# Kernel optimization log

Hardware: AMD Instinct MI355X
Metric: run time of the kernel (lower is better)

The kernel has to match this reference:

```python
import jax, jax.numpy as jnp
import numpy as np

B_, H_, W_, C_ = 8, 56, 56, 96
D_ = int(C_ * 2.0)          # d_inner = 192
N_ = 16                     # d_state
K_ = 4                      # scan directions
R_ = (C_ + 15) // 16        # dt_rank 'auto' = 6
MLP_H = 4 * C_
EPS = 1e-5


def setup_inputs() -> dict:
    key = jax.random.key(0)
    ks = jax.random.split(key, 16)
    s = 0.02
    rn = lambda k, sh, sc=1.0: jax.random.normal(k, sh, dtype=jnp.float32) * sc
    return dict(
        x=rn(ks[0], (B_, H_, W_, C_)),
        ln1_w=jnp.ones((C_,), jnp.float32), ln1_b=jnp.zeros((C_,), jnp.float32),
        in_proj_w=rn(ks[1], (2 * D_, C_), s),
        conv_w=rn(ks[2], (D_, 1, 3, 3), s), conv_b=jnp.zeros((D_,), jnp.float32),
        x_proj_w=rn(ks[3], (K_, R_ + 2 * N_, D_), s),
        dt_proj_w=rn(ks[4], (K_, D_, R_), s),
        dt_proj_b=rn(ks[5], (K_, D_), 0.1),
        A_logs=jax.random.uniform(ks[6], (K_ * D_, N_), jnp.float32, 0.0, 3.0),
        Ds=jnp.ones((K_ * D_,), jnp.float32),
        out_norm_w=jnp.ones((D_,), jnp.float32), out_norm_b=jnp.zeros((D_,), jnp.float32),
        out_proj_w=rn(ks[7], (C_, D_), s),
        ln2_w=jnp.ones((C_,), jnp.float32), ln2_b=jnp.zeros((C_,), jnp.float32),
        fc1_w=rn(ks[8], (MLP_H, C_), s), fc1_b=jnp.zeros((MLP_H,), jnp.float32),
        fc2_w=rn(ks[9], (C_, MLP_H), s), fc2_b=jnp.zeros((C_,), jnp.float32),
    )


def layer_norm(x, w, b):
    m = x.mean(-1, keepdims=True)
    v = ((x - m) ** 2).mean(-1, keepdims=True)
    return (x - m) / jnp.sqrt(v + EPS) * w + b


def ss2d(x, in_proj_w, conv_w, conv_b, x_proj_w, dt_proj_w, dt_proj_b,
         A_logs, Ds, out_norm_w, out_norm_b, out_proj_w):
    Bn, Hh, Ww, C = x.shape
    L = Hh * Ww
    xz = x @ in_proj_w.T                       # (B,H,W,2D)
    xc, z = jnp.split(xz, 2, axis=-1)
    xc = xc.transpose(0, 3, 1, 2)              # (B,D,H,W)
    xc = jax.lax.conv_general_dilated(xc, conv_w, (1, 1), 'SAME',
                                      feature_group_count=D_)
    xc = jax.nn.silu(xc + conv_b[None, :, None, None])
    # cross-scan: 4 traversal orders, each (B,D,L)
    x0 = xc.reshape(Bn, D_, L)
    x1 = xc.transpose(0, 1, 3, 2).reshape(Bn, D_, L)
    xs = jnp.stack([x0, x1, x0[..., ::-1], x1[..., ::-1]], axis=1)  # (B,K,D,L)
    xdbl = jnp.einsum('bkdl,kcd->bkcl', xs, x_proj_w)
    dts, Bs, Cs = jnp.split(xdbl, [R_, R_ + N_], axis=2)            # (B,K,R,L),(B,K,N,L)x2
    dts = jnp.einsum('bkrl,kdr->bkdl', dts, dt_proj_w)
    dts = jax.nn.softplus(dts + dt_proj_b[None, :, :, None])        # (B,K,D,L)
    A = -jnp.exp(A_logs).reshape(K_, D_, N_)                        # (K,D,N)

    def step(h, inp):
        xt, dtt, Bt, Ct = inp                  # (B,K,D),(B,K,D),(B,K,N),(B,K,N)
        h = h * jnp.exp(dtt[..., None] * A) + (dtt * xt)[..., None] * Bt[:, :, None, :]
        return h, jnp.einsum('bkdn,bkn->bkd', h, Ct)

    inps = (xs.transpose(3, 0, 1, 2), dts.transpose(3, 0, 1, 2),
            Bs.transpose(3, 0, 1, 2), Cs.transpose(3, 0, 1, 2))
    h0 = jnp.zeros((Bn, K_, D_, N_), jnp.float32)
    _, ys = jax.lax.scan(step, h0, inps)       # (L,B,K,D)
    ys = ys.transpose(1, 2, 3, 0)              # (B,K,D,L)
    ys = ys + Ds.reshape(K_, D_)[None, :, :, None] * xs
    # cross-merge: undo flips and transposed order
    y = ys[:, 0] + ys[:, 2, :, ::-1]
    y = y + (ys[:, 1] + ys[:, 3, :, ::-1]).reshape(Bn, D_, Ww, Hh) \
            .transpose(0, 1, 3, 2).reshape(Bn, D_, L)
    y = y.transpose(0, 2, 1).reshape(Bn, Hh, Ww, D_)
    y = layer_norm(y, out_norm_w, out_norm_b)
    y = y * jax.nn.silu(z)
    return y @ out_proj_w.T


def reference(x, ln1_w, ln1_b, in_proj_w, conv_w, conv_b, x_proj_w, dt_proj_w,
              dt_proj_b, A_logs, Ds, out_norm_w, out_norm_b, out_proj_w,
              ln2_w, ln2_b, fc1_w, fc1_b, fc2_w, fc2_b):
    # norm -> SS2D -> residual
    x = x + ss2d(layer_norm(x, ln1_w, ln1_b), in_proj_w, conv_w, conv_b,
                 x_proj_w, dt_proj_w, dt_proj_b, A_logs, Ds,
                 out_norm_w, out_norm_b, out_proj_w)
    # norm -> MLP -> residual
    h = layer_norm(x, ln2_w, ln2_b)
    h = jax.nn.gelu(h @ fc1_w.T + fc1_b) @ fc2_w.T + fc2_b
    return x + h
```

## Files before the change

kernel.cpp:

```cpp
#include <hip/hip_runtime.h>
#include <hip/hip_bf16.h>

typedef __hip_bfloat16 bf16;
typedef short bf16x8 __attribute__((ext_vector_type(8)));
typedef float f32x4 __attribute__((ext_vector_type(4)));

#define BBATCH 8
#define HHH 56
#define WWW 56
#define CCH 96
#define DIN 192
#define NST 16
#define KDIR 4
#define RDT 6
#define LLEN 3136
#define BLTOT 25088
#define SSEG 64
#define SEGL 49
#define PJC 38
#define PJW 152
#define PJS 40
#define PJS1 24
#define MLPH 384

#if defined(__has_builtin)
#if __has_builtin(__builtin_amdgcn_exp2f)
#define EXP2F(x) __builtin_amdgcn_exp2f(x)
#endif
#if __has_builtin(__builtin_amdgcn_logf)
#define LOG2F_(x) __builtin_amdgcn_logf(x)
#endif
#endif
#ifndef EXP2F
#define EXP2F(x) __expf((x) * 0.69314718056f)
#endif
#ifndef LOG2F_
#define LOG2F_(x) (__logf(x) * 1.44269504f)
#endif
#define LOG2E 1.44269504f

__device__ __forceinline__ float2 pk_mul(float2 a, float2 b) {
    float2 d;
    asm("v_pk_mul_f32 %0, %1, %2" : "=v"(d) : "v"(a), "v"(b));
    return d;
}
__device__ __forceinline__ float2 pk_fma(float2 a, float2 b, float2 c) {
    float2 d;
    asm("v_pk_fma_f32 %0, %1, %2, %3" : "=v"(d) : "v"(a), "v"(b), "v"(c));
    return d;
}

__device__ __forceinline__ float b2f(bf16 v) { return __bfloat162float(v); }
__device__ __forceinline__ bf16  f2b(float v) { return __float2bfloat16(v); }
__device__ __forceinline__ unsigned short f2bu(float f) {
    union { bf16 h; unsigned short u; } c; c.h = __float2bfloat16(f); return c.u;
}
__device__ __forceinline__ float bu2f(unsigned short u) {
    union { unsigned short u; bf16 h; } c; c.u = u; return __bfloat162float(c.h);
}
__device__ __forceinline__ float sigm(float x) { return 1.f / (1.f + __expf(-x)); }
__device__ __forceinline__ float softplusf(float x) {
    float t = EXP2F(-fabsf(x) * LOG2E);
    return fmaxf(x, 0.f) + 0.69314718f * LOG2F_(1.f + t);
}
__device__ __forceinline__ float geluf(float v) {
    float u = 0.7978845608028654f * (v + 0.044715f * v * v * v);
    float ey = __expf(2.f * u);
    float th = 1.f - 2.f / (ey + 1.f);
    return 0.5f * v * (1.f + th);
}

__device__ __forceinline__ int pos_map(int k, int l) {
    if (k & 2) l = LLEN - 1 - l;
    if (k & 1) { int q = l / WWW; int r = l - q * WWW; return r * WWW + q; }
    return l;
}

__global__ __launch_bounds__(256) void ln_rows(
    const float* __restrict__ xin, const float* __restrict__ w,
    const float* __restrict__ b, unsigned short* __restrict__ xn) {
    int row = blockIdx.x * 4 + (threadIdx.x >> 6);
    int lane = threadIdx.x & 63;
    const float* xr = xin + (size_t)row * 96;
    float2 v = make_float2(0.f, 0.f);
    if (lane < 48) v = *(const float2*)&xr[lane * 2];
    float s = v.x + v.y, s2 = v.x * v.x + v.y * v.y;
    for (int o = 32; o; o >>= 1) {
        s += __shfl_down(s, o);
        s2 += __shfl_down(s2, o);
    }
    s = __shfl(s, 0); s2 = __shfl(s2, 0);
    float m = s * (1.f / 96.f);
    float var = s2 * (1.f / 96.f) - m * m;
    float rs = rsqrtf(var + 1e-5f);
    if (lane < 48) {
        float o0 = (v.x - m) * rs * w[lane * 2] + b[lane * 2];
        float o1 = (v.y - m) * rs * w[lane * 2 + 1] + b[lane * 2 + 1];
        ushort2 u; u.x = f2bu(o0); u.y = f2bu(o1);
        *(ushort2*)&xn[(size_t)row * 96 + lane * 2] = u;
    }
}

template<int N, int K, int EPI>
__global__ __launch_bounds__(256) void gemm_mfma(
    const unsigned short* __restrict__ X, const float* __restrict__ W,
    const float* __restrict__ bias, const float* __restrict__ res,
    void* __restrict__ out0v, void* __restrict__ out1v) {
    __shared__ unsigned short a_sh[128 * 40];
    __shared__ unsigned short b_sh[64 * 40];
    const int t = threadIdx.x;
    const int P0 = blockIdx.x * 128;
    const int N0 = blockIdx.y * 64;
    const int w = t >> 6, lane = t & 63, q = lane >> 4, nl = lane & 15;
    f32x4 acc[2][4];
#pragma unroll
    for (int i = 0; i < 2; ++i)
#pragma unroll
        for (int j = 0; j < 4; ++j)
            acc[i][j] = (f32x4){0.f, 0.f, 0.f, 0.f};
    for (int k0 = 0; k0 < K; k0 += 32) {
        __syncthreads();
#pragma unroll
        for (int it = 0; it < 2; ++it) {
            int idx = t + it * 256;
            int pr = idx >> 2, kq = idx & 3;
            uint4 v = *(const uint4*)&X[(size_t)(P0 + pr) * K + k0 + kq * 8];
            *(uint4*)&a_sh[pr * 40 + kq * 8] = v;
        }
#pragma unroll
        for (int it = 0; it < 2; ++it) {
            int idx = t + it * 256;
            int nr = idx >> 3, kq = idx & 7;
            int ng = N0 + nr; if (ng > N - 1) ng = N - 1;
            float4 v = *(const float4*)&W[(size_t)ng * K + k0 + kq * 4];
            ushort4 u;
            u.x = f2bu(v.x); u.y = f2bu(v.y); u.z = f2bu(v.z); u.w = f2bu(v.w);
            *(ushort4*)&b_sh[nr * 40 + kq * 4] = u;
        }
        __syncthreads();
        bf16x8 af[2], bfr[4];
#pragma unroll
        for (int mf = 0; mf < 2; ++mf)
            af[mf] = *(const bf16x8*)&a_sh[(w * 32 + mf * 16 + nl) * 40 + q * 8];
#pragma unroll
        for (int nf = 0; nf < 4; ++nf)
            bfr[nf] = *(const bf16x8*)&b_sh[(nf * 16 + nl) * 40 + q * 8];
#pragma unroll
        for (int mf = 0; mf < 2; ++mf)
#pragma unroll
            for (int nf = 0; nf < 4; ++nf)
                acc[mf][nf] = __builtin_amdgcn_mfma_f32_16x16x32_bf16(
                    af[mf], bfr[nf], acc[mf][nf], 0, 0, 0);
    }
#pragma unroll
    for (int mf = 0; mf < 2; ++mf) {
#pragma unroll
        for (int nf = 0; nf < 4; ++nf) {
#pragma unroll
            for (int r = 0; r < 4; ++r) {
                float v = acc[mf][nf][r];
                size_t pos = (size_t)P0 + w * 32 + mf * 16 + q * 4 + r;
                int n = N0 + nf * 16 + nl;
                if constexpr (EPI == 0) {
                    unsigned short* xc = (unsigned short*)out0v;
                    unsigned short* zz = (unsigned short*)out1v;
                    if (n < 192) xc[pos * 192 + n] = f2bu(v);
                    else         zz[pos * 192 + (n - 192)] = f2bu(v);
                } else if constexpr (EPI == 1) {
                    if (n < 152) ((float*)out0v)[pos * 152 + n] = v;
                } else if constexpr (EPI == 2) {
                    if (n < 96) ((float*)out0v)[pos * 96 + n] = res[pos * 96 + n] + v;
                } else if constexpr (EPI == 3) {
                    ((unsigned short*)out0v)[pos * 384 + n] = f2bu(geluf(v + bias[n]));
                } else {
                    if (n < 96) ((float*)out0v)[pos * 96 + n] =
                        res[pos * 96 + n] + bias[n] + v;
                }
            }
        }
    }
}

__global__ __launch_bounds__(256) void k2_conv(
    const unsigned short* __restrict__ xcpre, const float* __restrict__ cw,
    const float* __restrict__ cb, unsigned short* __restrict__ xconv) {
    int idx = blockIdx.x * 256 + threadIdx.x;
    int dd = idx % 48;
    int P = idx / 48;
    int d0 = dd * 4;
    int b = P / LLEN, l = P - b * LLEN;
    int h = l / WWW, w = l - h * WWW;
    float acc0 = cb[d0], acc1 = cb[d0 + 1], acc2 = cb[d0 + 2], acc3 = cb[d0 + 3];
#pragma unroll
    for (int i = 0; i < 3; ++i) {
        int hh = h + i - 1;
        if (hh < 0 || hh >= HHH) continue;
#pragma unroll
        for (int j = 0; j < 3; ++j) {
            int ww = w + j - 1;
            if (ww < 0 || ww >= WWW) continue;
            ushort4 xv = *(const ushort4*)&xcpre[
                ((size_t)(b * LLEN + hh * WWW + ww)) * DIN + d0];
            acc0 = fmaf(bu2f(xv.x), cw[(d0 + 0) * 9 + i * 3 + j], acc0);
            acc1 = fmaf(bu2f(xv.y), cw[(d0 + 1) * 9 + i * 3 + j], acc1);
            acc2 = fmaf(bu2f(xv.z), cw[(d0 + 2) * 9 + i * 3 + j], acc2);
            acc3 = fmaf(bu2f(xv.w), cw[(d0 + 3) * 9 + i * 3 + j], acc3);
        }
    }
    acc0 = acc0 * sigm(acc0); acc1 = acc1 * sigm(acc1);
    acc2 = acc2 * sigm(acc2); acc3 = acc3 * sigm(acc3);
    ushort4 o;
    o.x = f2bu(acc0); o.y = f2bu(acc1); o.z = f2bu(acc2); o.w = f2bu(acc3);
    *(ushort4*)&xconv[(size_t)P * DIN + d0] = o;
}

__global__ __launch_bounds__(192) void k4_scan1(
    const bf16* __restrict__ xconv, const float* __restrict__ proj,
    const float* __restrict__ dtw, const float* __restrict__ dtb,
    const float* __restrict__ Alog, float* __restrict__ hloc,
    float* __restrict__ tsum) {
    __shared__ float pl[SEGL * PJS1];
    __shared__ int posl[SEGL];
    const int bid = blockIdx.x;
    const int s = bid & 63, k = (bid >> 6) & 3, b = bid >> 8;
    const int d = threadIdx.x;
    const int l0 = s * SEGL;
    for (int q = d; q < SEGL * 22; q += 192) {
        int st = q / 22, c = q - st * 22;
        int p = pos_map(k, l0 + st);
        int ofs = (c < 6) ? c : c + 2;
        pl[st * PJS1 + ofs] = proj[(size_t)(b * LLEN + p) * PJW + k * PJC + c];
    }
    if (d < SEGL) posl[d] = pos_map(k, l0 + d) * DIN;
    float w6[RDT];
#pragma unroll
    for (int r = 0; r < RDT; ++r) w6[r] = dtw[(k * DIN + d) * RDT + r];
    const float bias = dtb[k * DIN + d];
    float2 a2[8];
#pragma unroll
    for (int j = 0; j < 8; ++j) {
        a2[j].x = -__expf(Alog[(k * DIN + d) * NST + 2 * j]) * LOG2E;
        a2[j].y = -__expf(Alog[(k * DIN + d) * NST + 2 * j + 1]) * LOG2E;
    }
    float2 h2[8];
#pragma unroll
    for (int j = 0; j < 8; ++j) h2[j] = make_float2(0.f, 0.f);
    float T = 0.f;
    __syncthreads();
    const bf16* xg = xconv + (size_t)b * LLEN * DIN + d;
    for (int bt = 0; bt < 7; ++bt) {
        int off7[7]; float xv7[7];
#pragma unroll
        for (int i = 0; i < 7; ++i) off7[i] = posl[bt * 7 + i];
#pragma unroll
        for (int i = 0; i < 7; ++i) xv7[i] = b2f(xg[off7[i]]);
#pragma unroll
        for (int i = 0; i < 7; ++i) {
            const float* rowf = &pl[(bt * 7 + i) * PJS1];
            float4 g0 = *(const float4*)(rowf);
            float2 g1 = *(const float2*)(rowf + 4);
            float dtv = bias;
            dtv = fmaf(g0.x, w6[0], dtv); dtv = fmaf(g0.y, w6[1], dtv);
            dtv = fmaf(g0.z, w6[2], dtv); dtv = fmaf(g0.w, w6[3], dtv);
            dtv = fmaf(g1.x, w6[4], dtv); dtv = fmaf(g1.y, w6[5], dtv);
            dtv = softplusf(dtv);
            T += dtv;
            float2 dt2 = make_float2(dtv, dtv);
            float2 u2 = make_float2(dtv * xv7[i], dtv * xv7[i]);
#pragma unroll
            for (int g = 0; g < 4; ++g) {
                float4 Bv = *(const float4*)(rowf + 8 + 4 * g);
                float2 Blo = make_float2(Bv.x, Bv.y);
                float2 Bhi = make_float2(Bv.z, Bv.w);
                float2 alo = pk_mul(dt2, a2[2 * g]);
                float2 ahi = pk_mul(dt2, a2[2 * g + 1]);
                float2 elo, ehi;
                elo.x = EXP2F(alo.x); elo.y = EXP2F(alo.y);
                ehi.x = EXP2F(ahi.x); ehi.y = EXP2F(ahi.y);
                h2[2 * g]     = pk_fma(h2[2 * g],     elo, pk_mul(u2, Blo));
                h2[2 * g + 1] = pk_fma(h2[2 * g + 1], ehi, pk_mul(u2, Bhi));
            }
        }
    }
    size_t base = ((size_t)bid * DIN + d) * NST;
#pragma unroll
    for (int j = 0; j < 8; ++j) *(float2*)&hloc[base + 2 * j] = h2[j];
    tsum[bid * DIN + d] = T;
}

__global__ __launch_bounds__(256) void k5_carry(
    const float* hloc, const float* __restrict__ tsum,
    const float* __restrict__ Alog, float* hin) {
    int g = blockIdx.x * 256 + threadIdx.x;
    int n = g & 15;
    int dk = g >> 4;
    int d = dk % DIN;
    int bk = dk / DIN;
    int k = bk & 3;
    float a2 = -__expf(Alog[(k * DIN + d) * NST + n]) * LOG2E;
    float Hc = 0.f;
    for (int s = 0; s < SSEG; ++s) {
        int bid = bk * SSEG + s;
        size_t idx = ((size_t)bid * DIN + d) * NST + n;
        float hl = hloc[idx];
        float Tv = tsum[bid * DIN + d];
        hin[idx] = Hc;
        Hc = fmaf(EXP2F(a2 * Tv), Hc, hl);
    }
}

__global__ __launch_bounds__(192) void k6_scan2(
    const bf16* __restrict__ xconv, const float* __restrict__ proj,
    const float* __restrict__ dtw, const float* __restrict__ dtb,
    const float* __restrict__ Alog, const float* __restrict__ Dsp,
    const float* __restrict__ hin, bf16* __restrict__ ysm) {
    __shared__ float pl[SEGL * PJS];
    __shared__ int posl[SEGL];
    const int bid = blockIdx.x;
    const int s = bid & 63, k = (bid >> 6) & 3, b = bid >> 8;
    const int d = threadIdx.x;
    const int l0 = s * SEGL;
    for (int q = d; q < SEGL * PJC; q += 192) {
        int st = q / PJC, c = q - st * PJC;
        int p = pos_map(k, l0 + st);
        int ofs = (c < 6) ? c : c + 2;
        pl[st * PJS + ofs] = proj[(size_t)(b * LLEN + p) * PJW + k * PJC + c];
    }
    if (d < SEGL) posl[d] = pos_map(k, l0 + d) * DIN;
    float w6[RDT];
#pragma unroll
    for (int r = 0; r < RDT; ++r) w6[r] = dtw[(k * DIN + d) * RDT + r];
    const float bias = dtb[k * DIN + d];
    const float dsv = Dsp[k * DIN + d];
    float2 a2[8];
#pragma unroll
    for (int j = 0; j < 8; ++j) {
        a2[j].x = -__expf(Alog[(k * DIN + d) * NST + 2 * j]) * LOG2E;
        a2[j].y = -__expf(Alog[(k * DIN + d) * NST + 2 * j + 1]) * LOG2E;
    }
    float2 h2[8];
    size_t hbase = ((size_t)bid * DIN + d) * NST;
#pragma unroll
    for (int j = 0; j < 8; ++j) h2[j] = *(const float2*)&hin[hbase + 2 * j];
    __syncthreads();
    const bf16* xg = xconv + (size_t)b * LLEN * DIN + d;
    bf16* ysg = ysm + ((size_t)(b * KDIR + k) * LLEN) * DIN + d;
    for (int bt = 0; bt < 7; ++bt) {
        int off7[7]; float xv7[7];
#pragma unroll
        for (int i = 0; i < 7; ++i) off7[i] = posl[bt * 7 + i];
#pragma unroll
        for (int i = 0; i < 7; ++i) xv7[i] = b2f(xg[off7[i]]);
#pragma unroll
        for (int i = 0; i < 7; ++i) {
            const float* rowf = &pl[(bt * 7 + i) * PJS];
            float4 g0 = *(const float4*)(rowf);
            float2 g1 = *(const float2*)(rowf + 4);
            float dtv = bias;
            dtv = fmaf(g0.x, w6[0], dtv); dtv = fmaf(g0.y, w6[1], dtv);
            dtv = fmaf(g0.z, w6[2], dtv); dtv = fmaf(g0.w, w6[3], dtv);
            dtv = fmaf(g1.x, w6[4], dtv); dtv = fmaf(g1.y, w6[5], dtv);
            dtv = softplusf(dtv);
            float2 dt2 = make_float2(dtv, dtv);
            float2 u2 = make_float2(dtv * xv7[i], dtv * xv7[i]);
            float2 yac0 = make_float2(0.f, 0.f), yac1 = make_float2(0.f, 0.f);
#pragma unroll
            for (int g = 0; g < 4; ++g) {
                float4 Bv = *(const float4*)(rowf + 8 + 4 * g);
                float4 Cv = *(const float4*)(rowf + 24 + 4 * g);
                float2 Blo = make_float2(Bv.x, Bv.y);
                float2 Bhi = make_float2(Bv.z, Bv.w);
                float2 Clo = make_float2(Cv.x, Cv.y);
                float2 Chi = make_float2(Cv.z, Cv.w);
                float2 alo = pk_mul(dt2, a2[2 * g]);
                float2 ahi = pk_mul(dt2, a2[2 * g + 1]);
                float2 elo, ehi;
                elo.x = EXP2F(alo.x); elo.y = EXP2F(alo.y);
                ehi.x = EXP2F(ahi.x); ehi.y = EXP2F(ahi.y);
                h2[2 * g]     = pk_fma(h2[2 * g],     elo, pk_mul(u2, Blo));
                h2[2 * g + 1] = pk_fma(h2[2 * g + 1], ehi, pk_mul(u2, Bhi));
                yac0 = pk_fma(h2[2 * g],     Clo, yac0);
                yac1 = pk_fma(h2[2 * g + 1], Chi, yac1);
            }
            float y = (yac0.x + yac0.y) + (yac1.x + yac1.y);
            ysg[off7[i]] = f2b(fmaf(dsv, xv7[i], y));
        }
    }
}

__global__ __launch_bounds__(256) void k65_merge(
    const bf16* __restrict__ ysm, const bf16* __restrict__ z,
    const float* __restrict__ onw, const float* __restrict__ onb,
    bf16* __restrict__ ymod) {
    __shared__ float rb[16 * DIN];
    __shared__ float ps[256], pq[256];
    __shared__ float mrow[16], srow[16];
    const int t = threadIdx.x;
    const int P0 = blockIdx.x * 16;
    for (int q = t; q < 16 * DIN; q += 256) {
        int pos = q / DIN, c = q - pos * DIN;
        int P = P0 + pos;
        int b = P / LLEN, l = P - b * LLEN;
        size_t base = ((size_t)(b * KDIR) * LLEN + l) * DIN + c;
        size_t pstr = (size_t)LLEN * DIN;
        float v = b2f(ysm[base]) + b2f(ysm[base + pstr]) +
                  b2f(ysm[base + 2 * pstr]) + b2f(ysm[base + 3 * pstr]);
        rb[q] = v;
    }
    __syncthreads();
    {
        int pos = t >> 4, part = t & 15;
        float s = 0.f, s2 = 0.f;
        for (int i = 0; i < 12; ++i) {
            float v = rb[pos * DIN + part * 12 + i];
            s += v; s2 += v * v;
        }
        ps[pos * 16 + part] = s; pq[pos * 16 + part] = s2;
    }
    __syncthreads();
    if (t < 16) {
        float s = 0.f, s2 = 0.f;
        for (int i = 0; i < 16; ++i) { s += ps[t * 16 + i]; s2 += pq[t * 16 + i]; }
        float m = s * (1.f / DIN);
        float v = s2 * (1.f / DIN) - m * m;
        mrow[t] = m; srow[t] = rsqrtf(v + 1e-5f);
    }
    __syncthreads();
    for (int q = t; q < 16 * DIN; q += 256) {
        int pos = q / DIN, c = q - pos * DIN;
        int P = P0 + pos;
        float v = (rb[q] - mrow[pos]) * srow[pos] * onw[c] + onb[c];
        float zv = b2f(z[(size_t)P * DIN + c]);
        v *= zv * sigm(zv);
        ymod[(size_t)P * DIN + c] = f2b(v);
    }
}

extern "C" void kernel_launch(void* const* d_in, const int* in_sizes, int n_in,
                              void* d_out, int out_size, void* d_ws, size_t ws_size,
                              hipStream_t stream) {
    const float* x      = (const float*)d_in[0];
    const float* ln1w   = (const float*)d_in[1];
    const float* ln1b   = (const float*)d_in[2];
    const float* inpW   = (const float*)d_in[3];
    const float* convW  = (const float*)d_in[4];
    const float* convB  = (const float*)d_in[5];
    const float* xprojW = (const float*)d_in[6];
    const float* dtW    = (const float*)d_in[7];
    const float* dtB    = (const float*)d_in[8];
    const float* Alog   = (const float*)d_in[9];
    const float* Dsp    = (const float*)d_in[10];
    const float* onw    = (const float*)d_in[11];
    const float* onb    = (const float*)d_in[12];
    const float* outW   = (const float*)d_in[13];
    const float* ln2w   = (const float*)d_in[14];
    const float* ln2b   = (const float*)d_in[15];
    const float* fc1W   = (const float*)d_in[16];
    const float* fc1b   = (const float*)d_in[17];
    const float* fc2W   = (const float*)d_in[18];
    const float* fc2b   = (const float*)d_in[19];
    float* out = (float*)d_out;

    char* ws = (char*)d_ws;
    unsigned short* z_us    = (unsigned short*)(ws + 0);
    bf16*  z_bf             = (bf16*)z_us;
    bf16*  xconv_bf         = (bf16*)(ws + 9633792);
    float* proj_f           = (float*)(ws + 19267584);
    bf16*  ymod_bf          = (bf16*)(ws + 19267584);
    unsigned short* xn_us   = (unsigned short*)(ws + 34521088);
    float* tsum_f           = (float*)(ws + 34521088);
    unsigned short* xcpre_us= (unsigned short*)(ws + 39337984);
    float* hloc_f           = (float*)(ws + 48971776);
    float* hin_f            = hloc_f;
    float* y1_f             = (float*)(ws + 48971776);
    unsigned short* y1n_us  = (unsigned short*)(ws + 58605568);
    bf16*  ysm_bf           = (bf16*)(ws + 74137600);
    unsigned short* hmlp_us = (unsigned short*)(ws + 74137600);

    ln_rows<<<6272, 256, 0, stream>>>(x, ln1w, ln1b, xn_us);
    gemm_mfma<384, 96, 0><<<dim3(196, 6), 256, 0, stream>>>(
        xn_us, inpW, nullptr, nullptr, xcpre_us, z_us);
    k2_conv<<<4704, 256, 0, stream>>>(xcpre_us, convW, convB,
                                      (unsigned short*)xconv_bf);
    gemm_mfma<152, 192, 1><<<dim3(196, 3), 256, 0, stream>>>(
        (const unsigned short*)xconv_bf, xprojW, nullptr, nullptr, proj_f, nullptr);
    k4_scan1<<<2048, 192, 0, stream>>>(xconv_bf, proj_f, dtW, dtB, Alog, hloc_f, tsum_f);
    k5_carry<<<384, 256, 0, stream>>>(hloc_f, tsum_f, Alog, hin_f);
    k6_scan2<<<2048, 192, 0, stream>>>(xconv_bf, proj_f, dtW, dtB, Alog, Dsp, hin_f, ysm_bf);
    k65_merge<<<1568, 256, 0, stream>>>(ysm_bf, z_bf, onw, onb, ymod_bf);
    gemm_mfma<96, 192, 2><<<dim3(196, 2), 256, 0, stream>>>(
        (const unsigned short*)ymod_bf, outW, nullptr, x, y1_f, nullptr);
    ln_rows<<<6272, 256, 0, stream>>>(y1_f, ln2w, ln2b, y1n_us);
    gemm_mfma<384, 96, 3><<<dim3(196, 6), 256, 0, stream>>>(
        y1n_us, fc1W, fc1b, nullptr, hmlp_us, nullptr);
    gemm_mfma<96, 384, 4><<<dim3(196, 2), 256, 0, stream>>>(
        hmlp_us, fc2W, fc2b, y1_f, out, nullptr);
}
```

Measured before the change: 387.2 us.

## Split scan into more shorter segments and precompute A coefficients once

Raises the number of chunked-scan segments per sequence from 64 to 112 (28 steps each), so the two scan passes launch 3584 blocks instead of 2048 and fill more compute units with a shorter serial chain per block. A small pre-kernel computes -exp(A_log)*log2e once into workspace, and the scan and carry kernels load it instead of recomputing exponentials. Workspace offsets are reshuffled to fit the larger per-segment state buffers. In exchange, the serial carry kernel runs longer (112 steps) and the hloc/hin traffic grows with the segment count.

Result: faster. 379.5 us (-2.0%).

```diff
diff --git a/kernel.cpp b/kernel.cpp
--- a/kernel.cpp
+++ b/kernel.cpp
@@ -15,8 +15,8 @@
 #define RDT 6
 #define LLEN 3136
 #define BLTOT 25088
-#define SSEG 64
-#define SEGL 49
+#define SSEG 112
+#define SEGL 28
 #define PJC 38
 #define PJW 152
 #define PJS 40
@@ -74,6 +74,12 @@
     if (k & 2) l = LLEN - 1 - l;
     if (k & 1) { int q = l / WWW; int r = l - q * WWW; return r * WWW + q; }
     return l;
+}
+
+__global__ __launch_bounds__(256) void k0_pre(
+    const float* __restrict__ Alog, float* __restrict__ a2g) {
+    int i = blockIdx.x * 256 + threadIdx.x;
+    a2g[i] = -__expf(Alog[i]) * LOG2E;
 }
 
 __global__ __launch_bounds__(256) void ln_rows(
@@ -217,12 +223,14 @@
 __global__ __launch_bounds__(192) void k4_scan1(
     const bf16* __restrict__ xconv, const float* __restrict__ proj,
     const float* __restrict__ dtw, const float* __restrict__ dtb,
-    const float* __restrict__ Alog, float* __restrict__ hloc,
+    const float* __restrict__ a2g, float* __restrict__ hloc,
     float* __restrict__ tsum) {
     __shared__ float pl[SEGL * PJS1];
     __shared__ int posl[SEGL];
     const int bid = blockIdx.x;
-    const int s = bid & 63, k = (bid >> 6) & 3, b = bid >> 8;
+    const int s = bid % SSEG;
+    const int bk = bid / SSEG;
+    const int k = bk & 3, b = bk >> 2;
     const int d = threadIdx.x;
     const int l0 = s * SEGL;
     for (int q = d; q < SEGL * 22; q += 192) {
@@ -238,17 +246,15 @@
     const float bias = dtb[k * DIN + d];
     float2 a2[8];
 #pragma unroll
-    for (int j = 0; j < 8; ++j) {
-        a2[j].x = -__expf(Alog[(k * DIN + d) * NST + 2 * j]) * LOG2E;
-        a2[j].y = -__expf(Alog[(k * DIN + d) * NST + 2 * j + 1]) * LOG2E;
-    }
+    for (int j = 0; j < 8; ++j)
+        a2[j] = *(const float2*)&a2g[(k * DIN + d) * NST + 2 * j];
     float2 h2[8];
 #pragma unroll
     for (int j = 0; j < 8; ++j) h2[j] = make_float2(0.f, 0.f);
     float T = 0.f;
     __syncthreads();
     const bf16* xg = xconv + (size_t)b * LLEN * DIN + d;
-    for (int bt = 0; bt < 7; ++bt) {
+    for (int bt = 0; bt < 4; ++bt) {
         int off7[7]; float xv7[7];
 #pragma unroll
         for (int i = 0; i < 7; ++i) off7[i] = posl[bt * 7 + i];
@@ -290,14 +296,14 @@
 
 __global__ __launch_bounds__(256) void k5_carry(
     const float* hloc, const float* __restrict__ tsum,
-    const float* __restrict__ Alog, float* hin) {
+    const float* __restrict__ a2g, float* hin) {
     int g = blockIdx.x * 256 + threadIdx.x;
     int n = g & 15;
     int dk = g >> 4;
     int d = dk % DIN;
     int bk = dk / DIN;
     int k = bk & 3;
-    float a2 = -__expf(Alog[(k * DIN + d) * NST + n]) * LOG2E;
+    float a2 = a2g[(k * DIN + d) * NST + n];
     float Hc = 0.f;
     for (int s = 0; s < SSEG; ++s) {
         int bid = bk * SSEG + s;
@@ -312,12 +318,14 @@
 __global__ __launch_bounds__(192) void k6_scan2(
     const bf16* __restrict__ xconv, const float* __restrict__ proj,
     const float* __restrict__ dtw, const float* __restrict__ dtb,
-    const float* __restrict__ Alog, const float* __restrict__ Dsp,
+    const float* __restrict__ a2g, const float* __restrict__ Dsp,
     const float* __restrict__ hin, bf16* __restrict__ ysm) {
     __shared__ float pl[SEGL * PJS];
     __shared__ int posl[SEGL];
     const int bid = blockIdx.x;
-    const int s = bid & 63, k = (bid >> 6) & 3, b = bid >> 8;
+    const int s = bid % SSEG;
+    const int bk = bid / SSEG;
+    const int k = bk & 3, b = bk >> 2;
     const int d = threadIdx.x;
     const int l0 = s * SEGL;
     for (int q = d; q < SEGL * PJC; q += 192) {
@@ -334,18 +342,16 @@
     const float dsv = Dsp[k * DIN + d];
     float2 a2[8];
 #pragma unroll
-    for (int j = 0; j < 8; ++j) {
-        a2[j].x = -__expf(Alog[(k * DIN + d) * NST + 2 * j]) * LOG2E;
-        a2[j].y = -__expf(Alog[(k * DIN + d) * NST + 2 * j + 1]) * LOG2E;
-    }
+    for (int j = 0; j < 8; ++j)
+        a2[j] = *(const float2*)&a2g[(k * DIN + d) * NST + 2 * j];
     float2 h2[8];
     size_t hbase = ((size_t)bid * DIN + d) * NST;
 #pragma unroll
     for (int j = 0; j < 8; ++j) h2[j] = *(const float2*)&hin[hbase + 2 * j];
     __syncthreads();
     const bf16* xg = xconv + (size_t)b * LLEN * DIN + d;
-    bf16* ysg = ysm + ((size_t)(b * KDIR + k) * LLEN) * DIN + d;
-    for (int bt = 0; bt < 7; ++bt) {
+    bf16* ysg = ysm + ((size_t)bk * LLEN) * DIN + d;
+    for (int bt = 0; bt < 4; ++bt) {
         int off7[7]; float xv7[7];
 #pragma unroll
         for (int i = 0; i < 7; ++i) off7[i] = posl[bt * 7 + i];
@@ -470,13 +476,15 @@
     unsigned short* xn_us   = (unsigned short*)(ws + 34521088);
     float* tsum_f           = (float*)(ws + 34521088);
     unsigned short* xcpre_us= (unsigned short*)(ws + 39337984);
-    float* hloc_f           = (float*)(ws + 48971776);
+    float* hloc_f           = (float*)(ws + 39337984);
     float* hin_f            = hloc_f;
-    float* y1_f             = (float*)(ws + 48971776);
-    unsigned short* y1n_us  = (unsigned short*)(ws + 58605568);
-    bf16*  ysm_bf           = (bf16*)(ws + 74137600);
-    unsigned short* hmlp_us = (unsigned short*)(ws + 74137600);
-
+    float* y1_f             = (float*)(ws + 39337984);
+    unsigned short* y1n_us  = (unsigned short*)(ws + 48971776);
+    bf16*  ysm_bf           = (bf16*)(ws + 83378176);
+    unsigned short* hmlp_us = (unsigned short*)(ws + 83378176);
+    float* a2g_f            = (float*)(ws + 121913344);
+
+    k0_pre<<<48, 256, 0, stream>>>(Alog, a2g_f);
     ln_rows<<<6272, 256, 0, stream>>>(x, ln1w, ln1b, xn_us);
     gemm_mfma<384, 96, 0><<<dim3(196, 6), 256, 0, stream>>>(
         xn_us, inpW, nullptr, nullptr, xcpre_us, z_us);
@@ -484,9 +492,11 @@
                                       (unsigned short*)xconv_bf);
     gemm_mfma<152, 192, 1><<<dim3(196, 3), 256, 0, stream>>>(
         (const unsigned short*)xconv_bf, xprojW, nullptr, nullptr, proj_f, nullptr);
-    k4_scan1<<<2048, 192, 0, stream>>>(xconv_bf, proj_f, dtW, dtB, Alog, hloc_f, tsum_f);
-    k5_carry<<<384, 256, 0, stream>>>(hloc_f, tsum_f, Alog, hin_f);
-    k6_scan2<<<2048, 192, 0, stream>>>(xconv_bf, proj_f, dtW, dtB, Alog, Dsp, hin_f, ysm_bf);
+    k4_scan1<<<3584, 192, 0, stream>>>(xconv_bf, proj_f, dtW, dtB, a2g_f,
+                                       hloc_f, tsum_f);
+    k5_carry<<<384, 256, 0, stream>>>(hloc_f, tsum_f, a2g_f, hin_f);
+    k6_scan2<<<3584, 192, 0, stream>>>(xconv_bf, proj_f, dtW, dtB, a2g_f, Dsp,
+                                       hin_f, ysm_bf);
     k65_merge<<<1568, 256, 0, stream>>>(ysm_bf, z_bf, onw, onb, ymod_bf);
     gemm_mfma<96, 192, 2><<<dim3(196, 2), 256, 0, stream>>>(
         (const unsigned short*)ymod_bf, outW, nullptr, x, y1_f, nullptr);
```
